# Kernel tuning notes

Hardware: AMD Instinct MI355X
Metric: run time of the kernel (lower is better)

Reference implementation:

```python
import jax, jax.numpy as jnp
import numpy as np

B, N, D = 4, 2048, 512
M = 1024          # codebook_size
H, DH = 8, 64     # heads, dim_head
I = H * DH        # inner_dim = 512
FF = 1024         # dim_feedforward
EPS = 1e-5


def ln(x, g, b):
    mu = jnp.mean(x, axis=-1, keepdims=True)
    var = jnp.mean((x - mu) ** 2, axis=-1, keepdims=True)
    return (x - mu) * jax.lax.rsqrt(var + EPS) * g + b


def setup_inputs() -> dict:
    key = jax.random.key(0)
    ks = jax.random.split(key, 20)
    s = lambda fan: 1.0 / np.sqrt(fan)
    return {
        "context_input": jax.random.normal(ks[0], (B, N, D), jnp.float32),
        "context_mask": jax.random.randint(ks[1], (B, N), 0, 2) > 0,
        "codebook": jax.random.normal(ks[2], (M, D), jnp.float32),
        "norm_g": jnp.ones((D,)), "norm_b": jnp.zeros((D,)),
        "cnorm_g": jnp.ones((D,)), "cnorm_b": jnp.zeros((D,)),
        "wq": jax.random.normal(ks[3], (D, I)) * s(D),
        "wkv": jax.random.normal(ks[4], (D, 2 * I)) * s(D),
        "wo": jax.random.normal(ks[5], (I, D)) * s(I),
        "wo_b": jnp.zeros((D,)),
        "a_norm_g": jnp.ones((D,)), "a_norm_b": jnp.zeros((D,)),
        "a_qkv": jax.random.normal(ks[6], (D, 3 * I)) * s(D),
        "a_out": jax.random.normal(ks[7], (I, D)) * s(I),
        "f_norm_g": jnp.ones((D,)), "f_norm_b": jnp.zeros((D,)),
        "f_w1": jax.random.normal(ks[8], (D, FF)) * s(D),
        "f_w2": jax.random.normal(ks[9], (FF, D)) * s(FF),
    }


def _forward(context_input, context_mask, codebook, norm_g, norm_b, cnorm_g,
             cnorm_b, wq, wkv, wo, wo_b, a_norm_g, a_norm_b, a_qkv, a_out,
             f_norm_g, f_norm_b, f_w1, f_w2):
    scale = DH ** -0.5
    # ---- Vector quantization: nearest-codebook assignment (inference path) ----
    flat = context_input.reshape(-1, D)                      # [B*N, D]
    dist = (jnp.sum(flat ** 2, -1, keepdims=True)
            - 2.0 * flat @ codebook.T
            + jnp.sum(codebook ** 2, -1))                    # [B*N, M]
    flat_idx = jnp.argmin(dist, axis=-1)                     # [B*N]
    indices = flat_idx.reshape(B, N)
    quant = codebook[flat_idx]                               # [B*N, D]
    commit_loss = jnp.mean((flat - jax.lax.stop_gradient(quant)) ** 2)
    counts = jnp.zeros((M,), flat.dtype).at[flat_idx].add(1.0)
    probs = counts / flat_idx.shape[0]
    perplexity = jnp.exp(-jnp.sum(probs * jnp.log(probs + 1e-10)))
    # ---- Cross-attention: codebook queries attend over the context ----
    xq = ln(codebook, norm_g, norm_b)                        # [M, D]
    q = (xq @ wq).reshape(M, H, DH).transpose(1, 0, 2) * scale   # [H, M, DH]
    ctx = ln(context_input, cnorm_g, cnorm_b)                # [B, N, D]
    kv = ctx @ wkv                                           # [B, N, 2I]
    k, v = jnp.split(kv, 2, axis=-1)
    k = k.reshape(B, N, H, DH).transpose(0, 2, 1, 3)         # [B, H, N, DH]
    v = v.reshape(B, N, H, DH).transpose(0, 2, 1, 3)
    sim = jnp.einsum('hid,bhjd->bhij', q, k)                 # [B, H, M, N]
    big = jnp.finfo(sim.dtype).max
    sim = jnp.where(context_mask[:, None, None, :], sim, -big)
    attn = jax.nn.softmax(sim, axis=-1)
    out = jnp.einsum('bhij,bhjd->bhid', attn, v)             # [B, H, M, DH]
    out = out.transpose(0, 2, 1, 3).reshape(B, M, I) @ wo + wo_b  # [B, M, D]
    # ---- Transformer refinement layer (self-attn + FF, residual) ----
    h = ln(out, a_norm_g, a_norm_b)
    qkv = (h @ a_qkv).reshape(B, M, 3, H, DH)
    q2 = qkv[:, :, 0].transpose(0, 2, 1, 3) * scale
    k2 = qkv[:, :, 1].transpose(0, 2, 1, 3)
    v2 = qkv[:, :, 2].transpose(0, 2, 1, 3)
    a2 = jax.nn.softmax(jnp.einsum('bhid,bhjd->bhij', q2, k2), axis=-1)
    o2 = jnp.einsum('bhij,bhjd->bhid', a2, v2)
    out = out + o2.transpose(0, 2, 1, 3).reshape(B, M, I) @ a_out
    hf = ln(out, f_norm_g, f_norm_b)
    out = out + jax.nn.gelu(hf @ f_w1) @ f_w2
    # ---- Gather per-token outputs by VQ index ----
    outputs = jnp.take_along_axis(out, indices[:, :, None], axis=1)  # [B, N, D]
    return outputs, commit_loss, perplexity


def reference(context_input, context_mask, codebook, norm_g, norm_b, cnorm_g,
              cnorm_b, wq, wkv, wo, wo_b, a_norm_g, a_norm_b, a_qkv, a_out,
              f_norm_g, f_norm_b, f_w1, f_w2):
    return _forward(context_input, context_mask, codebook, norm_g, norm_b,
                    cnorm_g, cnorm_b, wq, wkv, wo, wo_b, a_norm_g, a_norm_b,
                    a_qkv, a_out, f_norm_g, f_norm_b, f_w1, f_w2)
```

## Files before the change

kernel.cpp:

```cpp
#include <hip/hip_runtime.h>
#include <math.h>

#define B_ 4
#define N_ 2048
#define D_ 512
#define M_ 1024
#define H_ 8
#define DH_ 64
#define I_ 512
#define FF_ 1024

typedef unsigned short u16;
typedef __attribute__((ext_vector_type(8))) short bf16x8;
typedef __attribute__((ext_vector_type(4))) float f32x4;

__device__ inline u16 f2b(float f) {
  union { float f; unsigned int u; } v; v.f = f;
  unsigned int u = v.u;
  u += 0x7fffu + ((u >> 16) & 1u);
  return (u16)(u >> 16);
}
__device__ inline float b2f(u16 h) {
  union { unsigned int u; float f; } v; v.u = ((unsigned int)h) << 16;
  return v.f;
}
__device__ inline float ex2(float x) { return __builtin_amdgcn_exp2f(x); }

__device__ inline float gelu_f(float x) {
  float x3 = x * x * x;
  return 0.5f * x * (1.f + tanhf(0.7978845608028654f * (x + 0.044715f * x3)));
}

__device__ inline bool better(float d1, int i1, float d2, int i2) {
  return d1 < d2 || (d1 == d2 && i1 < i2);
}
__device__ inline void cswap(float& da, int& ia, float& db, int& ib) {
  if (better(db, ib, da, ia)) {
    float td = da; da = db; db = td;
    int ti = ia; ia = ib; ib = ti;
  }
}
__device__ inline void kmin(float& da, int& ia, float db, int ib) {
  if (better(db, ib, da, ia)) { da = db; ia = ib; }
}

__global__ void zero_init_kernel(float* counts) {
  counts[threadIdx.x] = 0.f;
}

__global__ void mask_detect_kernel(const unsigned char* __restrict__ mb, int* flag) {
  __shared__ int any;
  if (threadIdx.x == 0) any = 0;
  __syncthreads();
  int acc = 0;
  for (int i = threadIdx.x; i < 8192; i += 256)
    if (i & 3) acc |= mb[i];
  if (acc) atomicOr(&any, 1);
  __syncthreads();
  if (threadIdx.x == 0) *flag = any;
}

__global__ void mask_norm_kernel(const void* __restrict__ mraw,
                                 const int* __restrict__ flag,
                                 int* __restrict__ mnorm) {
  int i = blockIdx.x * 256 + threadIdx.x;
  int v;
  if (*flag) v = ((const unsigned char*)mraw)[i];
  else       v = ((const int*)mraw)[i];
  mnorm[i] = (v != 0) ? 1 : 0;
}

__global__ __launch_bounds__(128) void code_sq_kernel(const float* __restrict__ cb,
                                                      double* __restrict__ csq,
                                                      float* __restrict__ csqf) {
  int row = blockIdx.x, tid = threadIdx.x;
  const float4* r4 = (const float4*)(cb + (size_t)row * D_);
  float4 v = r4[tid];
  double s = (double)v.x * v.x + (double)v.y * v.y + (double)v.z * v.z + (double)v.w * v.w;
  for (int off = 32; off; off >>= 1) s += __shfl_down(s, off);
  __shared__ double red[2];
  if ((tid & 63) == 0) red[tid >> 6] = s;
  __syncthreads();
  if (tid == 0) { csq[row] = red[0] + red[1]; csqf[row] = (float)(red[0] + red[1]); }
}

__global__ __launch_bounds__(256) void conv_bf16_kernel(const float* __restrict__ src,
                                                        u16* __restrict__ dst) {
  int i = (blockIdx.x * 256 + threadIdx.x) * 8;
  float4 a = *(const float4*)(src + i);
  float4 b = *(const float4*)(src + i + 4);
  uint4 o;
  o.x = (unsigned int)f2b(a.x) | ((unsigned int)f2b(a.y) << 16);
  o.y = (unsigned int)f2b(a.z) | ((unsigned int)f2b(a.w) << 16);
  o.z = (unsigned int)f2b(b.x) | ((unsigned int)f2b(b.y) << 16);
  o.w = (unsigned int)f2b(b.z) | ((unsigned int)f2b(b.w) << 16);
  *(uint4*)(dst + i) = o;
}

__global__ __launch_bounds__(256) void vq_top4_reduce_kernel(
    const float4* __restrict__ cand_part, int4* __restrict__ cand4)
{
  int t = blockIdx.x * 256 + threadIdx.x;
  float d0 = 1e30f, d1 = 1e30f, d2 = 1e30f, d3 = 1e30f;
  int x0 = 1 << 20, x1 = 1 << 21, x2 = 1 << 22, x3 = 1 << 23;
#pragma unroll
  for (int cb = 0; cb < 16; cb++) {
    float4 a = cand_part[(size_t)t * 32 + cb * 2];
    float4 b = cand_part[(size_t)t * 32 + cb * 2 + 1];
    float e0 = a.x, e1 = a.y, e2 = b.x, e3 = b.y;
    int y0 = __float_as_int(a.z), y1 = __float_as_int(a.w);
    int y2 = __float_as_int(b.z), y3 = __float_as_int(b.w);
    kmin(d0, x0, e3, y3); kmin(d1, x1, e2, y2);
    kmin(d2, x2, e1, y1); kmin(d3, x3, e0, y0);
    cswap(d0, x0, d2, x2); cswap(d1, x1, d3, x3);
    cswap(d0, x0, d1, x1); cswap(d2, x2, d3, x3);
  }
  cand4[t] = make_int4(x0, x1, x2, x3);
}

__global__ __launch_bounds__(256) void vq_refine4_kernel(
    const float* __restrict__ flat, const float* __restrict__ cb,
    const double* __restrict__ csq, const int4* __restrict__ cand4,
    int* __restrict__ out_idx, double* __restrict__ commit_partial,
    float* __restrict__ counts)
{
  int wave = threadIdx.x >> 6, lane = threadIdx.x & 63;
  int t = blockIdx.x * 4 + wave;
  int4 c = cand4[t];
  const float* x = flat + ((size_t)t << 9);
  const float* p0 = cb + ((size_t)c.x << 9);
  const float* p1 = cb + ((size_t)c.y << 9);
  const float* p2 = cb + ((size_t)c.z << 9);
  const float* p3 = cb + ((size_t)c.w << 9);
  double s0 = 0.0, s1 = 0.0, s2 = 0.0, s3 = 0.0, sx = 0.0;
#pragma unroll
  for (int i = 0; i < 8; i++) {
    int d = lane + i * 64;
    double xv = x[d];
    s0 += xv * (double)p0[d];
    s1 += xv * (double)p1[d];
    s2 += xv * (double)p2[d];
    s3 += xv * (double)p3[d];
    sx += xv * xv;
  }
  for (int off = 32; off; off >>= 1) {
    s0 += __shfl_down(s0, off);
    s1 += __shfl_down(s1, off);
    s2 += __shfl_down(s2, off);
    s3 += __shfl_down(s3, off);
    sx += __shfl_down(sx, off);
  }
  if (lane == 0) {
    double dd0 = csq[c.x] - 2.0 * s0;
    double dd1 = csq[c.y] - 2.0 * s1;
    double dd2 = csq[c.z] - 2.0 * s2;
    double dd3 = csq[c.w] - 2.0 * s3;
    int bi = c.x; double bd = dd0;
    if (dd1 < bd || (dd1 == bd && c.y < bi)) { bd = dd1; bi = c.y; }
    if (dd2 < bd || (dd2 == bd && c.z < bi)) { bd = dd2; bi = c.z; }
    if (dd3 < bd || (dd3 == bd && c.w < bi)) { bd = dd3; bi = c.w; }
    out_idx[t] = bi;
    commit_partial[t] = sx + bd;
    atomicAdd(counts + bi, 1.0f);
  }
}

__global__ __launch_bounds__(256) void ln_rows_kernel(
    const float* __restrict__ x, const float* __restrict__ g,
    const float* __restrict__ b, u16* __restrict__ y)
{
  int row = blockIdx.x, tid = threadIdx.x;
  const float* xr = x + (size_t)row * D_;
  float v0 = xr[tid], v1 = xr[tid + 256];
  float s = v0 + v1;
  for (int off = 32; off; off >>= 1) s += __shfl_down(s, off);
  __shared__ float red[4];
  __shared__ float bcast[2];
  if ((tid & 63) == 0) red[tid >> 6] = s;
  __syncthreads();
  if (tid == 0) bcast[0] = (red[0] + red[1] + red[2] + red[3]) * (1.f / 512.f);
  __syncthreads();
  float mu = bcast[0];
  float d0 = v0 - mu, d1 = v1 - mu;
  float q = d0 * d0 + d1 * d1;
  for (int off = 32; off; off >>= 1) q += __shfl_down(q, off);
  if ((tid & 63) == 0) red[tid >> 6] = q;
  __syncthreads();
  if (tid == 0) bcast[1] = rsqrtf((red[0] + red[1] + red[2] + red[3]) * (1.f / 512.f) + 1e-5f);
  __syncthreads();
  float rs = bcast[1];
  u16* yr = y + (size_t)row * D_;
  yr[tid]       = f2b(d0 * rs * g[tid] + b[tid]);
  yr[tid + 256] = f2b(d1 * rs * g[tid + 256] + b[tid + 256]);
}

struct WJobs {
  const float* src[7];
  u16* dst[7];
  int K[7], N[7], b0[8];
};

__global__ __launch_bounds__(256) void wconv_all_kernel(WJobs jobs) {
  __shared__ float tile[32][33];
  int bid = blockIdx.x;
  int j = 0;
#pragma unroll
  for (int i = 1; i < 7; i++) if (bid >= jobs.b0[i]) j = i;
  int tb = bid - jobs.b0[j];
  int K = jobs.K[j], Nn = jobs.N[j];
  int tiles_x = Nn >> 5;
  int n0 = (tb % tiles_x) << 5, k0 = (tb / tiles_x) << 5;
  const float* W = jobs.src[j];
  u16* WT = jobs.dst[j];
  int t = threadIdx.x;
  int ty = t >> 5, tx = t & 31;
#pragma unroll
  for (int i = 0; i < 4; i++)
    tile[ty + 8 * i][tx] = W[(size_t)(k0 + ty + 8 * i) * Nn + n0 + tx];
  __syncthreads();
#pragma unroll
  for (int i = 0; i < 4; i++)
    WT[(size_t)(n0 + ty + 8 * i) * K + k0 + tx] = f2b(tile[tx][ty + 8 * i]);
}

template <int BN>
__global__ __launch_bounds__(256, 4) void gemm_bf16_kernel(
    const u16* __restrict__ A, const u16* __restrict__ BT,
    const float* __restrict__ bias, const float* __restrict__ resid,
    float* __restrict__ Cf, u16* __restrict__ Cb,
    const float* __restrict__ csqf, float4* __restrict__ cand_part,
    int M, int N, int K, int act)
{
  constexpr int MF = (BN == 128) ? 4 : 2;
  constexpr int ROWS_W = (BN == 128) ? 64 : 32;
  __shared__ __attribute__((aligned(16))) u16 As[2][128 * 40];
  __shared__ __attribute__((aligned(16))) u16 Bs[2][BN * 40];
  int tid = threadIdx.x;
  int lane = tid & 63, wave = tid >> 6;
  int wr = (BN == 128) ? (wave >> 1) : wave;
  int wc = (BN == 128) ? (wave & 1) : 0;
  int nwgx = gridDim.x;
  int nwg = nwgx * gridDim.y;
  int flat = blockIdx.y * nwgx + blockIdx.x;
  if ((nwg & 7) == 0) flat = (flat & 7) * (nwg >> 3) + (flat >> 3);
  int row0 = (flat / nwgx) << 7, col0 = (flat % nwgx) * BN;
  int l15 = lane & 15, l4 = lane >> 4;
  int sr = tid >> 2, skc = tid & 3;
  int soff = sr * 40 + skc * 8;
  const u16* pA0 = A + (size_t)(row0 + sr) * K + skc * 8;
  const u16* pA1 = A + (size_t)(row0 + 64 + sr) * K + skc * 8;
  const u16* pB0 = BT + (size_t)(col0 + sr) * K + skc * 8;
  const u16* pB1 = (BN == 128) ? (BT + (size_t)(col0 + 64 + sr) * K + skc * 8) : nullptr;
  f32x4 acc[MF][4] = {};
  int KT = K >> 5;
  bf16x8 ra0 = *(const bf16x8*)pA0;
  bf16x8 ra1 = *(const bf16x8*)pA1;
  bf16x8 rb0 = *(const bf16x8*)pB0;
  bf16x8 rb1;
  if constexpr (BN == 128) rb1 = *(const bf16x8*)pB1;
  *(bf16x8*)&As[0][soff] = ra0;
  *(bf16x8*)&As[0][64 * 40 + soff] = ra1;
  *(bf16x8*)&Bs[0][soff] = rb0;
  if constexpr (BN == 128) *(bf16x8*)&Bs[0][64 * 40 + soff] = rb1;
  if (KT > 1) {
    ra0 = *(const bf16x8*)(pA0 + 32);
    ra1 = *(const bf16x8*)(pA1 + 32);
    rb0 = *(const bf16x8*)(pB0 + 32);
    if constexpr (BN == 128) rb1 = *(const bf16x8*)(pB1 + 32);
  }
  for (int kt = 0; kt < KT; kt++) {
    int cur = kt & 1;
    __syncthreads();
    if (kt + 1 < KT) {
      *(bf16x8*)&As[cur ^ 1][soff] = ra0;
      *(bf16x8*)&As[cur ^ 1][64 * 40 + soff] = ra1;
      *(bf16x8*)&Bs[cur ^ 1][soff] = rb0;
      if constexpr (BN == 128) *(bf16x8*)&Bs[cur ^ 1][64 * 40 + soff] = rb1;
    }
    if (kt + 2 < KT) {
      int ko = (kt + 2) << 5;
      ra0 = *(const bf16x8*)(pA0 + ko);
      ra1 = *(const bf16x8*)(pA1 + ko);
      rb0 = *(const bf16x8*)(pB0 + ko);
      if constexpr (BN == 128) rb1 = *(const bf16x8*)(pB1 + ko);
    }
    bf16x8 af[MF], bfr[4];
#pragma unroll
    for (int m = 0; m < MF; m++)
      af[m] = *(const bf16x8*)&As[cur][(wr * ROWS_W + m * 16 + l15) * 40 + l4 * 8];
#pragma unroll
    for (int n = 0; n < 4; n++)
      bfr[n] = *(const bf16x8*)&Bs[cur][(wc * 64 + n * 16 + l15) * 40 + l4 * 8];
#pragma unroll
    for (int m = 0; m < MF; m++)
#pragma unroll
      for (int n = 0; n < 4; n++)
        acc[m][n] = __builtin_amdgcn_mfma_f32_16x16x32_bf16(af[m], bfr[n], acc[m][n], 0, 0, 0);
  }
  if constexpr (BN == 128) {
    if (act == 2) {
      float csq_l[4];
#pragma unroll
      for (int n = 0; n < 4; n++) csq_l[n] = csqf[col0 + wc * 64 + n * 16 + l15];
      int cbase = col0 + wc * 64 + l15;
      int slot = ((col0 >> 7) << 1) + wc;
#pragma unroll
      for (int m = 0; m < 4; m++) {
#pragma unroll
        for (int r = 0; r < 4; r++) {
          float d0 = csq_l[0] - 2.f * acc[m][0][r];
          float d1 = csq_l[1] - 2.f * acc[m][1][r];
          float d2 = csq_l[2] - 2.f * acc[m][2][r];
          float d3 = csq_l[3] - 2.f * acc[m][3][r];
          int x0 = cbase, x1 = cbase + 16, x2 = cbase + 32, x3 = cbase + 48;
          cswap(d0, x0, d1, x1); cswap(d2, x2, d3, x3);
          cswap(d0, x0, d2, x2); cswap(d1, x1, d3, x3);
          cswap(d1, x1, d2, x2);
          for (int off = 1; off < 16; off <<= 1) {
            float e0 = __shfl_xor(d0, off), e1 = __shfl_xor(d1, off);
            float e2 = __shfl_xor(d2, off), e3 = __shfl_xor(d3, off);
            int y0 = __shfl_xor(x0, off), y1 = __shfl_xor(x1, off);
            int y2 = __shfl_xor(x2, off), y3 = __shfl_xor(x3, off);
            kmin(d0, x0, e3, y3); kmin(d1, x1, e2, y2);
            kmin(d2, x2, e1, y1); kmin(d3, x3, e0, y0);
            cswap(d0, x0, d2, x2); cswap(d1, x1, d3, x3);
            cswap(d0, x0, d1, x1); cswap(d2, x2, d3, x3);
          }
          if (l15 == 0) {
            int row = row0 + wr * 64 + m * 16 + l4 * 4 + r;
            float4 v1, v2;
            v1.x = d0; v1.y = d1;
            v1.z = __int_as_float(x0); v1.w = __int_as_float(x1);
            v2.x = d2; v2.y = d3;
            v2.z = __int_as_float(x2); v2.w = __int_as_float(x3);
            cand_part[(size_t)row * 32 + slot * 2]     = v1;
            cand_part[(size_t)row * 32 + slot * 2 + 1] = v2;
          }
        }
      }
      return;
    }
  }
#pragma unroll
  for (int m = 0; m < MF; m++) {
#pragma unroll
    for (int n = 0; n < 4; n++) {
      int col = col0 + wc * 64 + n * 16 + l15;
      float bv = bias ? bias[col] : 0.f;
#pragma unroll
      for (int r = 0; r < 4; r++) {
        int row = row0 + wr * ROWS_W + m * 16 + l4 * 4 + r;
        float v = acc[m][n][r] + bv;
        if (act == 1) v = gelu_f(v);
        if (resid) v += resid[(size_t)row * N + col];
        if (Cf) Cf[(size_t)row * N + col] = v;
        if (Cb) Cb[(size_t)row * N + col] = f2b(v);
      }
    }
  }
}

__global__ __launch_bounds__(256) void vt_kernel(
    const u16* __restrict__ src, size_t b_stride, int row_stride, int col0,
    int n_rows, u16* __restrict__ dst)
{
  __shared__ __attribute__((aligned(16))) u16 tile[32][72];
  int t = threadIdx.x;
  int bh = blockIdx.y;
  int b = bh >> 3, h = bh & 7;
  int n0 = blockIdx.x * 32;
  int n = t >> 3, dc = t & 7;
  *(bf16x8*)&tile[n][dc * 8] =
      *(const bf16x8*)(src + (size_t)b * b_stride + (size_t)(n0 + n) * row_stride + col0 + h * 64 + dc * 8);
  __syncthreads();
  int d = t >> 2, ns = t & 3;
  bf16x8 o;
#pragma unroll
  for (int i = 0; i < 8; i++) o[i] = (short)tile[ns * 8 + i][d];
  *(bf16x8*)(dst + ((size_t)bh * 64 + d) * n_rows + n0 + ns * 8) = o;
}

__global__ __launch_bounds__(256, 4) void attn_mfma_kernel(
    const u16* __restrict__ Q, size_t q_bs, int q_stride,
    const u16* __restrict__ Kp, size_t k_bs, int k_stride, int k_extra,
    const u16* __restrict__ Vt, const int* __restrict__ mask,
    float scale, float* __restrict__ Opart, float* __restrict__ MLpart,
    int n_keys)
{
  __shared__ __attribute__((aligned(16))) u16 Ks[8 * 64 * 8];
  __shared__ __attribute__((aligned(16))) u16 Vs[8 * 64 * 8];
  __shared__ __attribute__((aligned(16))) u16 Ps[4][8 * 16 * 8];
  __shared__ float mbias[64];
  int tid = threadIdx.x, lane = tid & 63, wave = tid >> 6;
  int flat = blockIdx.x + (blockIdx.y << 4) + (blockIdx.z << 7);
  int swz = ((flat & 7) << 7) + (flat >> 3);
  int qb = swz & 15, h = (swz >> 4) & 7, z = swz >> 7;
  int b = z & 3, split = z >> 2;
  int q0 = qb * 64 + wave * 16;
  int l15 = lane & 15, l4 = lane >> 4;
  int nh = n_keys >> 1;
  int nstart = split * nh, nend = nstart + nh;

  const u16* qrow = Q + (size_t)b * q_bs + (size_t)(q0 + l15) * q_stride + h * 64 + l4 * 8;
  bf16x8 qf0 = *(const bf16x8*)qrow;
  bf16x8 qf1 = *(const bf16x8*)(qrow + 32);
  f32x4 o_acc[4] = {};
  float m_run = -3.0e38f, l_run = 0.f;
  int srow = tid >> 2, schunk = tid & 3;
  const u16* kbase = Kp + (size_t)b * k_bs + k_extra + h * 64;
  const u16* vtbase = Vt + (size_t)(b * 8 + h) * 64 * n_keys;

  bf16x8 pk0, pk1, pv0, pv1;
  int pmv = 1;
  {
    const u16* krow = kbase + (size_t)(nstart + srow) * k_stride;
    pk0 = *(const bf16x8*)(krow + schunk * 8);
    pk1 = *(const bf16x8*)(krow + (schunk + 4) * 8);
    const u16* vrow = vtbase + (size_t)srow * n_keys + nstart;
    pv0 = *(const bf16x8*)(vrow + schunk * 8);
    pv1 = *(const bf16x8*)(vrow + (schunk + 4) * 8);
    if (mask && tid < 64) pmv = mask[(size_t)b * n_keys + nstart + tid];
  }

  for (int n0 = nstart; n0 < nend; n0 += 64) {
    __syncthreads();
    *(bf16x8*)&Ks[(schunk * 64 + srow) * 8]       = pk0;
    *(bf16x8*)&Ks[((schunk + 4) * 64 + srow) * 8] = pk1;
    *(bf16x8*)&Vs[(schunk * 64 + srow) * 8]       = pv0;
    *(bf16x8*)&Vs[((schunk + 4) * 64 + srow) * 8] = pv1;
    if (tid < 64) mbias[tid] = (mask && !pmv) ? -3.0e38f : 0.f;
    __syncthreads();
    if (n0 + 64 < nend) {
      const u16* krow = kbase + (size_t)(n0 + 64 + srow) * k_stride;
      pk0 = *(const bf16x8*)(krow + schunk * 8);
      pk1 = *(const bf16x8*)(krow + (schunk + 4) * 8);
      const u16* vrow = vtbase + (size_t)srow * n_keys + n0 + 64;
      pv0 = *(const bf16x8*)(vrow + schunk * 8);
      pv1 = *(const bf16x8*)(vrow + (schunk + 4) * 8);
      if (mask && tid < 64) pmv = mask[(size_t)b * n_keys + n0 + 64 + tid];
    }
    f32x4 sac[4];
#pragma unroll
    for (int kb = 0; kb < 4; kb++) {
      bf16x8 kf0 = *(const bf16x8*)&Ks[(l4 * 64 + kb * 16 + l15) * 8];
      bf16x8 kf1 = *(const bf16x8*)&Ks[((l4 + 4) * 64 + kb * 16 + l15) * 8];
      f32x4 zz = {};
      zz = __builtin_amdgcn_mfma_f32_16x16x32_bf16(kf0, qf0, zz, 0, 0, 0);
      sac[kb] = __builtin_amdgcn_mfma_f32_16x16x32_bf16(kf1, qf1, zz, 0, 0, 0);
    }
    float sv[16];
    float pmax = -3.0e38f;
#pragma unroll
    for (int kb = 0; kb < 4; kb++) {
      float4 bs = *(const float4*)&mbias[kb * 16 + l4 * 4];
      sv[kb * 4 + 0] = fmaf(sac[kb][0], scale, bs.x);
      sv[kb * 4 + 1] = fmaf(sac[kb][1], scale, bs.y);
      sv[kb * 4 + 2] = fmaf(sac[kb][2], scale, bs.z);
      sv[kb * 4 + 3] = fmaf(sac[kb][3], scale, bs.w);
#pragma unroll
      for (int r = 0; r < 4; r++) pmax = fmaxf(pmax, sv[kb * 4 + r]);
    }
    pmax = fmaxf(pmax, __shfl_xor(pmax, 16));
    pmax = fmaxf(pmax, __shfl_xor(pmax, 32));
    if (!__all(pmax - m_run <= 11.5f)) {
      float mnew = fmaxf(m_run, pmax);
      float al = ex2(m_run - mnew);
      l_run *= al;
      m_run = mnew;
      float alr[4];
#pragma unroll
      for (int r = 0; r < 4; r++) alr[r] = __shfl(al, l4 * 4 + r, 64);
#pragma unroll
      for (int nb = 0; nb < 4; nb++)
#pragma unroll
        for (int r = 0; r < 4; r++) o_acc[nb][r] *= alr[r];
    }
    float psum = 0.f;
    u16 pb[16];
#pragma unroll
    for (int i = 0; i < 16; i++) {
      float p = ex2(sv[i] - m_run);
      psum += p;
      pb[i] = f2b(p);
    }
    psum += __shfl_xor(psum, 16);
    psum += __shfl_xor(psum, 32);
    l_run += psum;
#pragma unroll
    for (int kb = 0; kb < 4; kb++) {
      uint2 w;
      w.x = (unsigned int)pb[kb * 4 + 0] | ((unsigned int)pb[kb * 4 + 1] << 16);
      w.y = (unsigned int)pb[kb * 4 + 2] | ((unsigned int)pb[kb * 4 + 3] << 16);
      *(uint2*)&Ps[wave][((kb * 2 + (l4 >> 1)) * 16 + l15) * 8 + (l4 & 1) * 4] = w;
    }
#pragma unroll
    for (int c = 0; c < 2; c++) {
      bf16x8 pf = *(const bf16x8*)&Ps[wave][((c * 4 + l4) * 16 + l15) * 8];
#pragma unroll
      for (int nb = 0; nb < 4; nb++) {
        bf16x8 vf = *(const bf16x8*)&Vs[((c * 4 + l4) * 64 + nb * 16 + l15) * 8];
        o_acc[nb] = __builtin_amdgcn_mfma_f32_16x16x32_bf16(pf, vf, o_acc[nb], 0, 0, 0);
      }
    }
  }
  int pr_base = ((split * 4 + b) * 8 + h) * 1024;
#pragma unroll
  for (int nb = 0; nb < 4; nb++)
#pragma unroll
    for (int r = 0; r < 4; r++)
      Opart[(size_t)(pr_base + q0 + l4 * 4 + r) * 64 + nb * 16 + l15] = o_acc[nb][r];
  if (lane < 16) {
    int pr = pr_base + q0 + lane;
    MLpart[2 * pr]     = m_run;
    MLpart[2 * pr + 1] = l_run;
  }
}

__global__ __launch_bounds__(256) void attn_combine_kernel(
    const float* __restrict__ Opart, const float* __restrict__ MLpart,
    u16* __restrict__ O, size_t o_bs)
{
  int idx = blockIdx.x * 256 + threadIdx.x;
  int d = idx & 63, gq = idx >> 6;
  int row = gq & 1023, bh = gq >> 10;
  int h = bh & 7, b = bh >> 3;
  float m0 = MLpart[2 * gq], l0 = MLpart[2 * gq + 1];
  float m1 = MLpart[2 * (32768 + gq)], l1 = MLpart[2 * (32768 + gq) + 1];
  float mmax = fmaxf(m0, m1);
  float w0 = ex2(m0 - mmax), w1 = ex2(m1 - mmax);
  float l = l0 * w0 + l1 * w1;
  float o = Opart[(size_t)gq * 64 + d] * w0 + Opart[(size_t)(32768 + gq) * 64 + d] * w1;
  O[(size_t)b * o_bs + (size_t)row * 512 + h * 64 + d] = f2b(o / l);
}

__global__ __launch_bounds__(128) void gather_kernel(
    const float* __restrict__ x2, const int* __restrict__ idx, float* __restrict__ out)
{
  int t = blockIdx.x;
  int b = t >> 11;
  int code = idx[t];
  const float4* src = (const float4*)(x2 + ((size_t)(b * M_ + code) << 9));
  float4* dst = (float4*)(out + ((size_t)t << 9));
  dst[threadIdx.x] = src[threadIdx.x];
}

__global__ void scalars_kernel(const float* __restrict__ counts,
                               const double* __restrict__ commit_partial,
                               float* __restrict__ out_tail)
{
  int tid = threadIdx.x;
  double cs = 0.0;
#pragma unroll
  for (int i = 0; i < 8; i++) cs += commit_partial[tid + i * 1024];
  double p = (double)counts[tid] / 8192.0;
  double e = p * log(p + 1e-10);
  for (int off = 32; off; off >>= 1) {
    cs += __shfl_down(cs, off);
    e  += __shfl_down(e, off);
  }
  __shared__ double redc[16], rede[16];
  if ((tid & 63) == 0) { redc[tid >> 6] = cs; rede[tid >> 6] = e; }
  __syncthreads();
  if (tid == 0) {
    double sc = 0.0, se = 0.0;
    for (int i = 0; i < 16; i++) { sc += redc[i]; se += rede[i]; }
    out_tail[0] = (float)(sc / (8192.0 * 512.0));
    out_tail[1] = (float)exp(-se);
  }
}

extern "C" void kernel_launch(void* const* d_in, const int* in_sizes, int n_in,
                              void* d_out, int out_size, void* d_ws, size_t ws_size,
                              hipStream_t stream) {
  const float* ctx      = (const float*)d_in[0];
  const void*  mask_raw = d_in[1];
  const float* codebook = (const float*)d_in[2];
  const float* norm_g   = (const float*)d_in[3];
  const float* norm_b   = (const float*)d_in[4];
  const float* cnorm_g  = (const float*)d_in[5];
  const float* cnorm_b  = (const float*)d_in[6];
  const float* wq       = (const float*)d_in[7];
  const float* wkv      = (const float*)d_in[8];
  const float* wo       = (const float*)d_in[9];
  const float* wo_b     = (const float*)d_in[10];
  const float* a_norm_g = (const float*)d_in[11];
  const float* a_norm_b = (const float*)d_in[12];
  const float* a_qkv    = (const float*)d_in[13];
  const float* a_out    = (const float*)d_in[14];
  const float* f_norm_g = (const float*)d_in[15];
  const float* f_norm_b = (const float*)d_in[16];
  const float* f_w1     = (const float*)d_in[17];
  const float* f_w2     = (const float*)d_in[18];
  float* out = (float*)d_out;
  const float LOG2E = 1.4426950408889634f;

  char* ws = (char*)d_ws;
  int*    mask_flag  = (int*)(ws + 64);
  float*  counts     = (float*)(ws + 128);
  double* code_sq    = (double*)(ws + 4224);
  float*  csqf       = (float*)(ws + 12416);
  int*    indices    = (int*)(ws + 16512);
  int*    mask_norm  = (int*)(ws + 49280);
  int4*   cand4      = (int4*)(ws + 82048);
  double* commit_partial = (double*)(ws + 262144);
  float*  attn_ml    = (float*)(ws + 524288);

  char* pool = ws + (1 << 20);
  u16*   vqA  = (u16*)(pool);
  u16*   vqBT = (u16*)(pool + ((size_t)26 << 20));
  float4* cand_part = (float4*)(pool + ((size_t)30 << 20));
  char* regA  = pool;
  char* regB  = pool + ((size_t)16 << 20);
  char* regC  = pool + ((size_t)24 << 20);
  char* regD  = pool + ((size_t)32 << 20);
  char* regE  = pool + ((size_t)40 << 20);
  char* regF  = pool + ((size_t)44 << 20);
  size_t woff = (1 << 20) + ((size_t)64 << 20);
  u16* wqT    = (u16*)(ws + woff); woff += (size_t)512 * 512 * 2;
  u16* wkvT   = (u16*)(ws + woff); woff += (size_t)1024 * 512 * 2;
  u16* woT    = (u16*)(ws + woff); woff += (size_t)512 * 512 * 2;
  u16* aqkvT  = (u16*)(ws + woff); woff += (size_t)1536 * 512 * 2;
  u16* aoutT  = (u16*)(ws + woff); woff += (size_t)512 * 512 * 2;
  u16* fw1T   = (u16*)(ws + woff); woff += (size_t)1024 * 512 * 2;
  u16* fw2T   = (u16*)(ws + woff); woff += (size_t)512 * 1024 * 2;
  u16* xq_b   = (u16*)(ws + woff); woff += (size_t)1024 * 512 * 2;
  u16* qs_b   = (u16*)(ws + woff); woff += (size_t)1024 * 512 * 2;

  u16* kv_b     = (u16*)regA;
  u16* qkv2_b   = (u16*)regA;
  u16* ctx_ln_b = (u16*)regB;
  u16* VtS      = (u16*)regB;
  u16* VtX      = (u16*)regC;
  float* x1_f   = (float*)regC;
  float* x0_f   = (float*)regD;
  u16* att_out_b = (u16*)regE;
  u16* h_b       = (u16*)regE;
  u16* o2_b      = (u16*)regE;
  u16* hf_b      = (u16*)regE;
  u16* g_b      = (u16*)regF;
  float* x2_f   = (float*)(pool + ((size_t)52 << 20));
  float* attn_part = (float*)regF;

  zero_init_kernel<<<1, 1024, 0, stream>>>(counts);
  mask_detect_kernel<<<1, 256, 0, stream>>>((const unsigned char*)mask_raw, mask_flag);
  mask_norm_kernel<<<32, 256, 0, stream>>>(mask_raw, mask_flag, mask_norm);
  code_sq_kernel<<<1024, 128, 0, stream>>>(codebook, code_sq, csqf);
  conv_bf16_kernel<<<2048, 256, 0, stream>>>(ctx, vqA);
  conv_bf16_kernel<<<256, 256, 0, stream>>>(codebook, vqBT);
  gemm_bf16_kernel<128><<<dim3(8, 64), 256, 0, stream>>>(vqA, vqBT, nullptr, nullptr,
                                                    nullptr, nullptr, csqf, cand_part,
                                                    8192, 1024, 512, 2);
  vq_top4_reduce_kernel<<<32, 256, 0, stream>>>(cand_part, cand4);
  vq_refine4_kernel<<<2048, 256, 0, stream>>>(ctx, codebook, code_sq, cand4, indices,
                                              commit_partial, counts);

  WJobs jobs;
  jobs.src[0] = wq;    jobs.dst[0] = wqT;   jobs.K[0] = 512;  jobs.N[0] = 512;
  jobs.src[1] = wkv;   jobs.dst[1] = wkvT;  jobs.K[1] = 512;  jobs.N[1] = 1024;
  jobs.src[2] = wo;    jobs.dst[2] = woT;   jobs.K[2] = 512;  jobs.N[2] = 512;
  jobs.src[3] = a_qkv; jobs.dst[3] = aqkvT; jobs.K[3] = 512;  jobs.N[3] = 1536;
  jobs.src[4] = a_out; jobs.dst[4] = aoutT; jobs.K[4] = 512;  jobs.N[4] = 512;
  jobs.src[5] = f_w1;  jobs.dst[5] = fw1T;  jobs.K[5] = 512;  jobs.N[5] = 1024;
  jobs.src[6] = f_w2;  jobs.dst[6] = fw2T;  jobs.K[6] = 1024; jobs.N[6] = 512;
  int acc_b = 0;
  for (int i = 0; i < 7; i++) {
    jobs.b0[i] = acc_b;
    acc_b += (jobs.K[i] >> 5) * (jobs.N[i] >> 5);
  }
  jobs.b0[7] = acc_b;
  wconv_all_kernel<<<acc_b, 256, 0, stream>>>(jobs);

  ln_rows_kernel<<<1024, 256, 0, stream>>>(codebook, norm_g, norm_b, xq_b);
  gemm_bf16_kernel<64><<<dim3(8, 8), 256, 0, stream>>>(xq_b, wqT, nullptr, nullptr,
                                                   nullptr, qs_b, nullptr, nullptr,
                                                   1024, 512, 512, 0);
  ln_rows_kernel<<<8192, 256, 0, stream>>>(ctx, cnorm_g, cnorm_b, ctx_ln_b);
  gemm_bf16_kernel<128><<<dim3(8, 64), 256, 0, stream>>>(ctx_ln_b, wkvT, nullptr, nullptr,
                                                    nullptr, kv_b, nullptr, nullptr,
                                                    8192, 1024, 512, 0);
  vt_kernel<<<dim3(64, 32), 256, 0, stream>>>(kv_b, (size_t)2048 * 1024, 1024, 512, 2048, VtX);
  attn_mfma_kernel<<<dim3(16, 8, 8), 256, 0, stream>>>(
      qs_b, 0, 512, kv_b, (size_t)2048 * 1024, 1024, 0, VtX, mask_norm,
      0.125f * LOG2E, attn_part, attn_ml, 2048);
  attn_combine_kernel<<<8192, 256, 0, stream>>>(attn_part, attn_ml, att_out_b, (size_t)1024 * 512);
  gemm_bf16_kernel<64><<<dim3(8, 32), 256, 0, stream>>>(att_out_b, woT, wo_b, nullptr,
                                                    x0_f, nullptr, nullptr, nullptr,
                                                    4096, 512, 512, 0);

  ln_rows_kernel<<<4096, 256, 0, stream>>>(x0_f, a_norm_g, a_norm_b, h_b);
  gemm_bf16_kernel<64><<<dim3(24, 32), 256, 0, stream>>>(h_b, aqkvT, nullptr, nullptr,
                                                     nullptr, qkv2_b, nullptr, nullptr,
                                                     4096, 1536, 512, 0);
  vt_kernel<<<dim3(32, 32), 256, 0, stream>>>(qkv2_b, (size_t)1024 * 1536, 1536, 1024, 1024, VtS);
  attn_mfma_kernel<<<dim3(16, 8, 8), 256, 0, stream>>>(
      qkv2_b, (size_t)1024 * 1536, 1536, qkv2_b, (size_t)1024 * 1536, 1536, 512, VtS, nullptr,
      0.125f * LOG2E, attn_part, attn_ml, 1024);
  attn_combine_kernel<<<8192, 256, 0, stream>>>(attn_part, attn_ml, o2_b, (size_t)1024 * 512);
  gemm_bf16_kernel<64><<<dim3(8, 32), 256, 0, stream>>>(o2_b, aoutT, nullptr, x0_f,
                                                    x1_f, nullptr, nullptr, nullptr,
                                                    4096, 512, 512, 0);
  ln_rows_kernel<<<4096, 256, 0, stream>>>(x1_f, f_norm_g, f_norm_b, hf_b);
  gemm_bf16_kernel<64><<<dim3(16, 32), 256, 0, stream>>>(hf_b, fw1T, nullptr, nullptr,
                                                    nullptr, g_b, nullptr, nullptr,
                                                    4096, 1024, 512, 1);
  gemm_bf16_kernel<64><<<dim3(8, 32), 256, 0, stream>>>(g_b, fw2T, nullptr, x1_f,
                                                    x2_f, nullptr, nullptr, nullptr,
                                                    4096, 512, 1024, 0);

  gather_kernel<<<8192, 128, 0, stream>>>(x2_f, indices, out);
  scalars_kernel<<<1, 1024, 0, stream>>>(counts, commit_partial, out + (size_t)B_ * N_ * D_);
}
```

Baseline: 316.7 us.

## Process two query tiles per wave, split keys four ways, store partials in bf16

Each attention wave now handles 32 query rows (two 16-row tiles) against every K/V tile it loads into shared memory, so the K/V staging cost is shared by twice as many queries. The key range is split into four parts instead of two to keep the grid the same size, and the combine kernel merges four partials. Partial outputs are stored as bf16 rather than fp32 to cut partial-result traffic, and the workspace layout is moved to fit. The cost is higher register pressure per wave and some loss of precision in the partial sums.

```diff
diff --git a/kernel.cpp b/kernel.cpp
--- a/kernel.cpp
+++ b/kernel.cpp
@@ -384,28 +384,31 @@
     const u16* __restrict__ Q, size_t q_bs, int q_stride,
     const u16* __restrict__ Kp, size_t k_bs, int k_stride, int k_extra,
     const u16* __restrict__ Vt, const int* __restrict__ mask,
-    float scale, float* __restrict__ Opart, float* __restrict__ MLpart,
+    float scale, u16* __restrict__ Opart, float* __restrict__ MLpart,
     int n_keys)
 {
   __shared__ __attribute__((aligned(16))) u16 Ks[8 * 64 * 8];
   __shared__ __attribute__((aligned(16))) u16 Vs[8 * 64 * 8];
-  __shared__ __attribute__((aligned(16))) u16 Ps[4][8 * 16 * 8];
+  __shared__ __attribute__((aligned(16))) u16 Ps[4][8 * 32 * 8];
   __shared__ float mbias[64];
   int tid = threadIdx.x, lane = tid & 63, wave = tid >> 6;
-  int flat = blockIdx.x + (blockIdx.y << 4) + (blockIdx.z << 7);
+  int flat = blockIdx.x + (blockIdx.y << 3) + (blockIdx.z << 6);
   int swz = ((flat & 7) << 7) + (flat >> 3);
-  int qb = swz & 15, h = (swz >> 4) & 7, z = swz >> 7;
+  int qb = swz & 7, h = (swz >> 3) & 7, z = swz >> 6;
   int b = z & 3, split = z >> 2;
-  int q0 = qb * 64 + wave * 16;
+  int q0 = qb * 128 + wave * 32;
   int l15 = lane & 15, l4 = lane >> 4;
-  int nh = n_keys >> 1;
-  int nstart = split * nh, nend = nstart + nh;
+  int nq = n_keys >> 2;
+  int nstart = split * nq, nend = nstart + nq;
 
   const u16* qrow = Q + (size_t)b * q_bs + (size_t)(q0 + l15) * q_stride + h * 64 + l4 * 8;
-  bf16x8 qf0 = *(const bf16x8*)qrow;
-  bf16x8 qf1 = *(const bf16x8*)(qrow + 32);
-  f32x4 o_acc[4] = {};
-  float m_run = -3.0e38f, l_run = 0.f;
+  bf16x8 qfA0 = *(const bf16x8*)qrow;
+  bf16x8 qfA1 = *(const bf16x8*)(qrow + 32);
+  const u16* qrowB = qrow + 16 * q_stride;
+  bf16x8 qfB0 = *(const bf16x8*)qrowB;
+  bf16x8 qfB1 = *(const bf16x8*)(qrowB + 32);
+  f32x4 oA[4] = {}, oB[4] = {};
+  float mA = -3.0e38f, lA = 0.f, mB = -3.0e38f, lB = 0.f;
   int srow = tid >> 2, schunk = tid & 3;
   const u16* kbase = Kp + (size_t)b * k_bs + k_extra + h * 64;
   const u16* vtbase = Vt + (size_t)(b * 8 + h) * 64 * n_keys;
@@ -439,67 +442,118 @@
       pv1 = *(const bf16x8*)(vrow + (schunk + 4) * 8);
       if (mask && tid < 64) pmv = mask[(size_t)b * n_keys + n0 + 64 + tid];
     }
-    f32x4 sac[4];
+    f32x4 sacA[4], sacB[4];
 #pragma unroll
     for (int kb = 0; kb < 4; kb++) {
       bf16x8 kf0 = *(const bf16x8*)&Ks[(l4 * 64 + kb * 16 + l15) * 8];
       bf16x8 kf1 = *(const bf16x8*)&Ks[((l4 + 4) * 64 + kb * 16 + l15) * 8];
-      f32x4 zz = {};
-      zz = __builtin_amdgcn_mfma_f32_16x16x32_bf16(kf0, qf0, zz, 0, 0, 0);
-      sac[kb] = __builtin_amdgcn_mfma_f32_16x16x32_bf16(kf1, qf1, zz, 0, 0, 0);
-    }
-    float sv[16];
-    float pmax = -3.0e38f;
-#pragma unroll
-    for (int kb = 0; kb < 4; kb++) {
-      float4 bs = *(const float4*)&mbias[kb * 16 + l4 * 4];
-      sv[kb * 4 + 0] = fmaf(sac[kb][0], scale, bs.x);
-      sv[kb * 4 + 1] = fmaf(sac[kb][1], scale, bs.y);
-      sv[kb * 4 + 2] = fmaf(sac[kb][2], scale, bs.z);
-      sv[kb * 4 + 3] = fmaf(sac[kb][3], scale, bs.w);
-#pragma unroll
-      for (int r = 0; r < 4; r++) pmax = fmaxf(pmax, sv[kb * 4 + r]);
-    }
-    pmax = fmaxf(pmax, __shfl_xor(pmax, 16));
-    pmax = fmaxf(pmax, __shfl_xor(pmax, 32));
-    if (!__all(pmax - m_run <= 11.5f)) {
-      float mnew = fmaxf(m_run, pmax);
-      float al = ex2(m_run - mnew);
-      l_run *= al;
-      m_run = mnew;
-      float alr[4];
-#pragma unroll
-      for (int r = 0; r < 4; r++) alr[r] = __shfl(al, l4 * 4 + r, 64);
-#pragma unroll
-      for (int nb = 0; nb < 4; nb++)
-#pragma unroll
-        for (int r = 0; r < 4; r++) o_acc[nb][r] *= alr[r];
-    }
-    float psum = 0.f;
-    u16 pb[16];
-#pragma unroll
-    for (int i = 0; i < 16; i++) {
-      float p = ex2(sv[i] - m_run);
-      psum += p;
-      pb[i] = f2b(p);
-    }
-    psum += __shfl_xor(psum, 16);
-    psum += __shfl_xor(psum, 32);
-    l_run += psum;
-#pragma unroll
-    for (int kb = 0; kb < 4; kb++) {
-      uint2 w;
-      w.x = (unsigned int)pb[kb * 4 + 0] | ((unsigned int)pb[kb * 4 + 1] << 16);
-      w.y = (unsigned int)pb[kb * 4 + 2] | ((unsigned int)pb[kb * 4 + 3] << 16);
-      *(uint2*)&Ps[wave][((kb * 2 + (l4 >> 1)) * 16 + l15) * 8 + (l4 & 1) * 4] = w;
+      f32x4 za = {}, zb = {};
+      za = __builtin_amdgcn_mfma_f32_16x16x32_bf16(kf0, qfA0, za, 0, 0, 0);
+      sacA[kb] = __builtin_amdgcn_mfma_f32_16x16x32_bf16(kf1, qfA1, za, 0, 0, 0);
+      zb = __builtin_amdgcn_mfma_f32_16x16x32_bf16(kf0, qfB0, zb, 0, 0, 0);
+      sacB[kb] = __builtin_amdgcn_mfma_f32_16x16x32_bf16(kf1, qfB1, zb, 0, 0, 0);
+    }
+    {
+      float pmax = -3.0e38f;
+#pragma unroll
+      for (int kb = 0; kb < 4; kb++) {
+        float4 bs = *(const float4*)&mbias[kb * 16 + l4 * 4];
+        sacA[kb][0] = fmaf(sacA[kb][0], scale, bs.x);
+        sacA[kb][1] = fmaf(sacA[kb][1], scale, bs.y);
+        sacA[kb][2] = fmaf(sacA[kb][2], scale, bs.z);
+        sacA[kb][3] = fmaf(sacA[kb][3], scale, bs.w);
+#pragma unroll
+        for (int r = 0; r < 4; r++) pmax = fmaxf(pmax, sacA[kb][r]);
+      }
+      pmax = fmaxf(pmax, __shfl_xor(pmax, 16));
+      pmax = fmaxf(pmax, __shfl_xor(pmax, 32));
+      if (!__all(pmax - mA <= 11.5f)) {
+        float mnew = fmaxf(mA, pmax);
+        float al = ex2(mA - mnew);
+        lA *= al;
+        mA = mnew;
+        float alr[4];
+#pragma unroll
+        for (int r = 0; r < 4; r++) alr[r] = __shfl(al, l4 * 4 + r, 64);
+#pragma unroll
+        for (int nb = 0; nb < 4; nb++)
+#pragma unroll
+          for (int r = 0; r < 4; r++) oA[nb][r] *= alr[r];
+      }
+      float psum = 0.f;
+#pragma unroll
+      for (int kb = 0; kb < 4; kb++) {
+        u16 pb[4];
+#pragma unroll
+        for (int r = 0; r < 4; r++) {
+          float p = ex2(sacA[kb][r] - mA);
+          psum += p;
+          pb[r] = f2b(p);
+        }
+        uint2 w;
+        w.x = (unsigned int)pb[0] | ((unsigned int)pb[1] << 16);
+        w.y = (unsigned int)pb[2] | ((unsigned int)pb[3] << 16);
+        *(uint2*)&Ps[wave][((kb * 2 + (l4 >> 1)) * 32 + l15) * 8 + (l4 & 1) * 4] = w;
+      }
+      psum += __shfl_xor(psum, 16);
+      psum += __shfl_xor(psum, 32);
+      lA += psum;
+    }
+    {
+      float pmax = -3.0e38f;
+#pragma unroll
+      for (int kb = 0; kb < 4; kb++) {
+        float4 bs = *(const float4*)&mbias[kb * 16 + l4 * 4];
+        sacB[kb][0] = fmaf(sacB[kb][0], scale, bs.x);
+        sacB[kb][1] = fmaf(sacB[kb][1], scale, bs.y);
+        sacB[kb][2] = fmaf(sacB[kb][2], scale, bs.z);
+        sacB[kb][3] = fmaf(sacB[kb][3], scale, bs.w);
+#pragma unroll
+        for (int r = 0; r < 4; r++) pmax = fmaxf(pmax, sacB[kb][r]);
+      }
+      pmax = fmaxf(pmax, __shfl_xor(pmax, 16));
+      pmax = fmaxf(pmax, __shfl_xor(pmax, 32));
+      if (!__all(pmax - mB <= 11.5f)) {
+        float mnew = fmaxf(mB, pmax);
+        float al = ex2(mB - mnew);
+        lB *= al;
+        mB = mnew;
+        float alr[4];
+#pragma unroll
+        for (int r = 0; r < 4; r++) alr[r] = __shfl(al, l4 * 4 + r, 64);
+#pragma unroll
+        for (int nb = 0; nb < 4; nb++)
+#pragma unroll
+          for (int r = 0; r < 4; r++) oB[nb][r] *= alr[r];
+      }
+      float psum = 0.f;
+#pragma unroll
+      for (int kb = 0; kb < 4; kb++) {
+        u16 pb[4];
+#pragma unroll
+        for (int r = 0; r < 4; r++) {
+          float p = ex2(sacB[kb][r] - mB);
+          psum += p;
+          pb[r] = f2b(p);
+        }
+        uint2 w;
+        w.x = (unsigned int)pb[0] | ((unsigned int)pb[1] << 16);
+        w.y = (unsigned int)pb[2] | ((unsigned int)pb[3] << 16);
+        *(uint2*)&Ps[wave][((kb * 2 + (l4 >> 1)) * 32 + 16 + l15) * 8 + (l4 & 1) * 4] = w;
+      }
+      psum += __shfl_xor(psum, 16);
+      psum += __shfl_xor(psum, 32);
+      lB += psum;
     }
 #pragma unroll
     for (int c = 0; c < 2; c++) {
-      bf16x8 pf = *(const bf16x8*)&Ps[wave][((c * 4 + l4) * 16 + l15) * 8];
+      bf16x8 pfA = *(const bf16x8*)&Ps[wave][((c * 4 + l4) * 32 + l15) * 8];
+      bf16x8 pfB = *(const bf16x8*)&Ps[wave][((c * 4 + l4) * 32 + 16 + l15) * 8];
 #pragma unroll
       for (int nb = 0; nb < 4; nb++) {
         bf16x8 vf = *(const bf16x8*)&Vs[((c * 4 + l4) * 64 + nb * 16 + l15) * 8];
-        o_acc[nb] = __builtin_amdgcn_mfma_f32_16x16x32_bf16(pf, vf, o_acc[nb], 0, 0, 0);
+        oA[nb] = __builtin_amdgcn_mfma_f32_16x16x32_bf16(pfA, vf, oA[nb], 0, 0, 0);
+        oB[nb] = __builtin_amdgcn_mfma_f32_16x16x32_bf16(pfB, vf, oB[nb], 0, 0, 0);
       }
     }
   }
@@ -507,30 +561,46 @@
 #pragma unroll
   for (int nb = 0; nb < 4; nb++)
 #pragma unroll
-    for (int r = 0; r < 4; r++)
-      Opart[(size_t)(pr_base + q0 + l4 * 4 + r) * 64 + nb * 16 + l15] = o_acc[nb][r];
+    for (int r = 0; r < 4; r++) {
+      Opart[(size_t)(pr_base + q0 + l4 * 4 + r) * 64 + nb * 16 + l15] = f2b(oA[nb][r]);
+      Opart[(size_t)(pr_base + q0 + 16 + l4 * 4 + r) * 64 + nb * 16 + l15] = f2b(oB[nb][r]);
+    }
   if (lane < 16) {
     int pr = pr_base + q0 + lane;
-    MLpart[2 * pr]     = m_run;
-    MLpart[2 * pr + 1] = l_run;
+    MLpart[2 * pr]     = mA;
+    MLpart[2 * pr + 1] = lA;
+  } else if (lane < 32) {
+    int pr = pr_base + q0 + 16 + l15;
+    MLpart[2 * pr]     = mB;
+    MLpart[2 * pr + 1] = lB;
   }
 }
 
 __global__ __launch_bounds__(256) void attn_combine_kernel(
-    const float* __restrict__ Opart, const float* __restrict__ MLpart,
+    const u16* __restrict__ Opart, const float* __restrict__ MLpart,
     u16* __restrict__ O, size_t o_bs)
 {
   int idx = blockIdx.x * 256 + threadIdx.x;
   int d = idx & 63, gq = idx >> 6;
   int row = gq & 1023, bh = gq >> 10;
   int h = bh & 7, b = bh >> 3;
-  float m0 = MLpart[2 * gq], l0 = MLpart[2 * gq + 1];
-  float m1 = MLpart[2 * (32768 + gq)], l1 = MLpart[2 * (32768 + gq) + 1];
-  float mmax = fmaxf(m0, m1);
-  float w0 = ex2(m0 - mmax), w1 = ex2(m1 - mmax);
-  float l = l0 * w0 + l1 * w1;
-  float o = Opart[(size_t)gq * 64 + d] * w0 + Opart[(size_t)(32768 + gq) * 64 + d] * w1;
-  O[(size_t)b * o_bs + (size_t)row * 512 + h * 64 + d] = f2b(o / l);
+  float m[4], l[4];
+  int pr[4];
+#pragma unroll
+  for (int s = 0; s < 4; s++) {
+    pr[s] = ((s * 4 + b) * 8 + h) * 1024 + row;
+    m[s] = MLpart[2 * pr[s]];
+    l[s] = MLpart[2 * pr[s] + 1];
+  }
+  float mmax = fmaxf(fmaxf(m[0], m[1]), fmaxf(m[2], m[3]));
+  float lsum = 0.f, osum = 0.f;
+#pragma unroll
+  for (int s = 0; s < 4; s++) {
+    float w = ex2(m[s] - mmax);
+    lsum += l[s] * w;
+    osum += b2f(Opart[(size_t)pr[s] * 64 + d]) * w;
+  }
+  O[(size_t)b * o_bs + (size_t)row * 512 + h * 64 + d] = f2b(osum / lsum);
 }
 
 __global__ __launch_bounds__(128) void gather_kernel(
@@ -603,12 +673,12 @@
   int*    mask_norm  = (int*)(ws + 49280);
   int4*   cand4      = (int4*)(ws + 82048);
   double* commit_partial = (double*)(ws + 262144);
-  float*  attn_ml    = (float*)(ws + 524288);
 
   char* pool = ws + (1 << 20);
   u16*   vqA  = (u16*)(pool);
-  u16*   vqBT = (u16*)(pool + ((size_t)26 << 20));
+  u16*   vqBT = (u16*)(pool + ((size_t)25 << 20));
   float4* cand_part = (float4*)(pool + ((size_t)30 << 20));
+  float* attn_ml = (float*)(pool + ((size_t)61 << 20));
   char* regA  = pool;
   char* regB  = pool + ((size_t)16 << 20);
   char* regC  = pool + ((size_t)24 << 20);
@@ -639,7 +709,7 @@
   u16* hf_b      = (u16*)regE;
   u16* g_b      = (u16*)regF;
   float* x2_f   = (float*)(pool + ((size_t)52 << 20));
-  float* attn_part = (float*)regF;
+  u16* attn_part = (u16*)regF;
 
   zero_init_kernel<<<1, 1024, 0, stream>>>(counts);
   mask_detect_kernel<<<1, 256, 0, stream>>>((const unsigned char*)mask_raw, mask_flag);
@@ -679,7 +749,7 @@
                                                     nullptr, kv_b, nullptr, nullptr,
                                                     8192, 1024, 512, 0);
   vt_kernel<<<dim3(64, 32), 256, 0, stream>>>(kv_b, (size_t)2048 * 1024, 1024, 512, 2048, VtX);
-  attn_mfma_kernel<<<dim3(16, 8, 8), 256, 0, stream>>>(
+  attn_mfma_kernel<<<dim3(8, 8, 16), 256, 0, stream>>>(
       qs_b, 0, 512, kv_b, (size_t)2048 * 1024, 1024, 0, VtX, mask_norm,
       0.125f * LOG2E, attn_part, attn_ml, 2048);
   attn_combine_kernel<<<8192, 256, 0, stream>>>(attn_part, attn_ml, att_out_b, (size_t)1024 * 512);
@@ -692,7 +762,7 @@
                                                      nullptr, qkv2_b, nullptr, nullptr,
                                                      4096, 1536, 512, 0);
   vt_kernel<<<dim3(32, 32), 256, 0, stream>>>(qkv2_b, (size_t)1024 * 1536, 1536, 1024, 1024, VtS);
-  attn_mfma_kernel<<<dim3(16, 8, 8), 256, 0, stream>>>(
+  attn_mfma_kernel<<<dim3(8, 8, 16), 256, 0, stream>>>(
       qkv2_b, (size_t)1024 * 1536, 1536, qkv2_b, (size_t)1024 * 1536, 1536, 512, VtS, nullptr,
       0.125f * LOG2E, attn_part, attn_ml, 1024);
   attn_combine_kernel<<<8192, 256, 0, stream>>>(attn_part, attn_ml, o2_b, (size_t)1024 * 512);
```

Result: no change. 316.4 us (-0.1%).
